# Kernel optimization log

Hardware: AMD Instinct MI355X
Metric: run time of the kernel (lower is better)

The kernel has to match this reference:

```python
import jax, jax.numpy as jnp
from jax import lax
import numpy as np

EPS = 1e-06


def _box_filter(x, radius):
    # Depthwise box mean with zero padding (matches F.conv2d padding=radius),
    # implemented separably: O(r) per pixel instead of O(r^2).
    C = x.shape[1]
    k = 2 * radius + 1
    dn = ('NCHW', 'OIHW', 'NCHW')
    kern_h = jnp.ones((C, 1, k, 1), x.dtype)
    kern_w = jnp.ones((C, 1, 1, k), x.dtype) / (k * k)
    y = lax.conv_general_dilated(x, kern_h, (1, 1), [(radius, radius), (0, 0)],
                                 feature_group_count=C, dimension_numbers=dn)
    return lax.conv_general_dilated(y, kern_w, (1, 1), [(0, 0), (radius, radius)],
                                    feature_group_count=C, dimension_numbers=dn)


def setup_inputs() -> dict:
    key = jax.random.key(0)
    k1, k2 = jax.random.split(key)
    I = jax.random.uniform(k1, (8, 1, 1024, 1024), dtype=jnp.float32)
    p = jax.random.uniform(k2, (8, 3, 1024, 1024), dtype=jnp.float32)
    return {"I": I, "p": p, "radius": 3}


def reference(I, p, radius):
    mean_I = _box_filter(I, radius)            # (B,1,H,W)
    mean_p = _box_filter(p, radius)            # (B,3,H,W)
    mean_Ip = _box_filter(I * p, radius)
    mean_II = _box_filter(I * I, radius)
    cov_Ip = mean_Ip - mean_I * mean_p
    var_I = mean_II - mean_I * mean_I
    a = cov_Ip / (var_I + EPS)
    b = mean_p - a * mean_I
    mean_a = _box_filter(a, radius)
    mean_b = _box_filter(b, radius)
    q = mean_a * I + mean_b
    return jnp.clip(q, 0.0, 1.0)
```

## Files before the change

### kernel.cpp

```cpp
#include <hip/hip_runtime.h>


typedef float v4 __attribute__((ext_vector_type(4)));
typedef float v2 __attribute__((ext_vector_type(2)));

#define TPB   64
#define OUTW  116
#define SEGH  32
#define HW    1024
#define NIDX  68
#define EPSF  1e-6f
#define INV49 (1.0f/49.0f)

struct St {
    v4 s14[2], s58[2];
    v4 t64[2]; v2 t62[2];
    v4 rab4[8][2]; v2 rab2[8][2];
    v2 rI[8];
    v4 ent[2][2];
    v2 lvp[3], lvpN[3];
};

template<int U>
__device__ __forceinline__ void rowStep(
    St& S, const int r, const int Yb, const int t, const int xc2,
    const bool ok0, const bool ok1, const bool sok, const int x0,
    const float* __restrict__ Ip, const float* __restrict__ P0,
    const float* __restrict__ P1, const float* __restrict__ P2,
    float* __restrict__ Q0, float* __restrict__ Q1, float* __restrict__ Q2,
    v4 (* __restrict__ c8)[2][2][NIDX],
    v4 (* __restrict__ c6A)[2][NIDX],
    v2 (* __restrict__ c6B)[2][NIDX])
{
    constexpr int SU  = U & 1;
    constexpr int WS  = U;
    constexpr int LS  = (U + 1) & 7;
    constexpr int IOS = (U + 2) & 7;

    {
        const v4 cE0 = S.ent[SU][0], cE1 = S.ent[SU][1];
        const v2 LI  = S.rI[LS];
        {
            const float Lx = LI.x;
            const float L0 = S.lvp[0].x, L1 = S.lvp[1].x, L2 = S.lvp[2].x;
            v4 d14, d58;
            d14.x = cE0.x - Lx;
            d14.y = cE0.x*cE0.x - Lx*Lx;
            d14.z = cE0.y - L0;
            d14.w = cE0.z - L1;
            d58.x = cE0.w - L2;
            d58.y = cE0.x*cE0.y - Lx*L0;
            d58.z = cE0.x*cE0.z - Lx*L1;
            d58.w = cE0.x*cE0.w - Lx*L2;
            S.s14[0] += d14; S.s58[0] += d58;
            c8[SU][0][0][t+2] = S.s14[0];
            c8[SU][0][1][t+2] = S.s58[0];
        }
        {
            const float Lx = LI.y;
            const float L0 = S.lvp[0].y, L1 = S.lvp[1].y, L2 = S.lvp[2].y;
            v4 d14, d58;
            d14.x = cE1.x - Lx;
            d14.y = cE1.x*cE1.x - Lx*Lx;
            d14.z = cE1.y - L0;
            d14.w = cE1.z - L1;
            d58.x = cE1.w - L2;
            d58.y = cE1.x*cE1.y - Lx*L0;
            d58.z = cE1.x*cE1.z - Lx*L1;
            d58.w = cE1.x*cE1.w - Lx*L2;
            S.s14[1] += d14; S.s58[1] += d58;
            c8[SU][1][0][t+2] = S.s14[1];
            c8[SU][1][1][t+2] = S.s58[1];
        }
        v2 nI; nI.x = cE0.x; nI.y = cE1.x;
        S.rI[WS] = nI;
    }
    asm volatile("" ::: "memory");

    {
        const v4 e14_1 = c8[SU][0][0][t+1], e14_2 = c8[SU][0][0][t+2],
                 e14_3 = c8[SU][0][0][t+3], e14_4 = c8[SU][0][0][t+4];
        const v4 o14_0 = c8[SU][1][0][t+0], o14_1 = c8[SU][1][0][t+1],
                 o14_2 = c8[SU][1][0][t+2], o14_3 = c8[SU][1][0][t+3];
        const v4 w14 = (e14_1 + e14_2 + e14_3) + (o14_1 + o14_2 + o14_3);
        v4 W14[2]; W14[0] = w14 + o14_0; W14[1] = w14 + e14_4;

        const v4 e58_1 = c8[SU][0][1][t+1], e58_2 = c8[SU][0][1][t+2],
                 e58_3 = c8[SU][0][1][t+3], e58_4 = c8[SU][0][1][t+4];
        const v4 o58_0 = c8[SU][1][1][t+0], o58_1 = c8[SU][1][1][t+1],
                 o58_2 = c8[SU][1][1][t+2], o58_3 = c8[SU][1][1][t+3];
        const v4 w58 = (e58_1 + e58_2 + e58_3) + (o58_1 + o58_2 + o58_3);
        v4 W58[2]; W58[0] = w58 + o58_0; W58[1] = w58 + e58_4;

        const int  yc   = Yb + r - 3;
        const bool ycok = (unsigned)yc < HW;
        const bool okc[2] = {ok0, ok1};
        #pragma unroll
        for (int c = 0; c < 2; ++c) {
            const v4 A = W14[c], B = W58[c];
            const float mi  = A.x * INV49;
            const float mii = A.y * INV49;
            const float rv  = __builtin_amdgcn_rcpf(mii - mi*mi + EPSF);
            const bool abok = ycok && okc[c];
            const float mp0 = A.z*INV49, mp1 = A.w*INV49, mp2 = B.x*INV49;
            const float a0 = (B.y*INV49 - mi*mp0)*rv;
            const float a1 = (B.z*INV49 - mi*mp1)*rv;
            const float a2 = (B.w*INV49 - mi*mp2)*rv;
            const float b0 = fmaf(-a0, mi, mp0);
            const float b1 = fmaf(-a1, mi, mp1);
            const float b2 = fmaf(-a2, mi, mp2);
            v4 ab4; ab4.x = abok?a0:0.f; ab4.y = abok?b0:0.f;
                    ab4.z = abok?a1:0.f; ab4.w = abok?b1:0.f;
            v2 ab2; ab2.x = abok?a2:0.f; ab2.y = abok?b2:0.f;
            S.t64[c] += ab4 - S.rab4[LS][c];  S.rab4[WS][c] = ab4;
            S.t62[c] += ab2 - S.rab2[LS][c];  S.rab2[WS][c] = ab2;
            c6A[SU][c][t+2] = S.t64[c];
            c6B[SU][c][t+2] = S.t62[c];
        }
    }
    asm volatile("" ::: "memory");

    {
        const int yE = Yb + r + 2;
        if (r <= 41 && (unsigned)yE < HW) {
            const size_t ro = (size_t)yE * HW + xc2;
            const v2 vI = *(const v2*)(Ip + ro);
            const v2 va = *(const v2*)(P0 + ro);
            const v2 vb = *(const v2*)(P1 + ro);
            const v2 vc = *(const v2*)(P2 + ro);
            v4 E0, E1;
            E0.x = ok0?vI.x:0.f; E0.y = ok0?va.x:0.f; E0.z = ok0?vb.x:0.f; E0.w = ok0?vc.x:0.f;
            E1.x = ok1?vI.y:0.f; E1.y = ok1?va.y:0.f; E1.z = ok1?vb.y:0.f; E1.w = ok1?vc.y:0.f;
            S.ent[SU][0] = E0; S.ent[SU][1] = E1;
        } else {
            const v4 z = {0.f,0.f,0.f,0.f};
            S.ent[SU][0] = z; S.ent[SU][1] = z;
        }
        const int yL = Yb + r - 6;
        if (r >= 6 && r <= 42 && (unsigned)yL < HW) {
            const size_t ro = (size_t)yL * HW + xc2;
            const v2 va = *(const v2*)(P0 + ro);
            const v2 vb = *(const v2*)(P1 + ro);
            const v2 vc = *(const v2*)(P2 + ro);
            v2 L0, L1v, L2v;
            L0.x  = ok0?va.x:0.f; L0.y  = ok1?va.y:0.f;
            L1v.x = ok0?vb.x:0.f; L1v.y = ok1?vb.y:0.f;
            L2v.x = ok0?vc.x:0.f; L2v.y = ok1?vc.y:0.f;
            S.lvpN[0] = L0; S.lvpN[1] = L1v; S.lvpN[2] = L2v;
        } else {
            const v2 z = {0.f,0.f};
            S.lvpN[0] = z; S.lvpN[1] = z; S.lvpN[2] = z;
        }
    }

    if ((unsigned)(r - 12) <= 31u) {
        const v4 eA1 = c6A[SU][0][t+1], eA2 = c6A[SU][0][t+2],
                 eA3 = c6A[SU][0][t+3], eA4 = c6A[SU][0][t+4];
        const v4 oA0 = c6A[SU][1][t+0], oA1 = c6A[SU][1][t+1],
                 oA2 = c6A[SU][1][t+2], oA3 = c6A[SU][1][t+3];
        const v2 eB1 = c6B[SU][0][t+1], eB2 = c6B[SU][0][t+2],
                 eB3 = c6B[SU][0][t+3], eB4 = c6B[SU][0][t+4];
        const v2 oB0 = c6B[SU][1][t+0], oB1 = c6B[SU][1][t+1],
                 oB2 = c6B[SU][1][t+2], oB3 = c6B[SU][1][t+3];
        const v4 wA = (eA1+eA2+eA3) + (oA1+oA2+oA3);
        const v2 wB = (eB1+eB2+eB3) + (oB1+oB2+oB3);
        const v4 A0 = wA + oA0, A1 = wA + eA4;
        const v2 B0 = wB + oB0, B1 = wB + eB4;
        if (sok) {
            const v2 io = S.rI[IOS];
            const int o = Yb + r - 6;
            const size_t ob = (size_t)o * HW + x0;
            v2 q;
            q.x = fminf(fmaxf(fmaf(A0.x*INV49, io.x, A0.y*INV49), 0.f), 1.f);
            q.y = fminf(fmaxf(fmaf(A1.x*INV49, io.y, A1.y*INV49), 0.f), 1.f);
            *(v2*)(Q0 + ob) = q;
            q.x = fminf(fmaxf(fmaf(A0.z*INV49, io.x, A0.w*INV49), 0.f), 1.f);
            q.y = fminf(fmaxf(fmaf(A1.z*INV49, io.y, A1.w*INV49), 0.f), 1.f);
            *(v2*)(Q1 + ob) = q;
            q.x = fminf(fmaxf(fmaf(B0.x*INV49, io.x, B0.y*INV49), 0.f), 1.f);
            q.y = fminf(fmaxf(fmaf(B1.x*INV49, io.y, B1.y*INV49), 0.f), 1.f);
            *(v2*)(Q2 + ob) = q;
        }
    }
    S.lvp[0] = S.lvpN[0]; S.lvp[1] = S.lvpN[1]; S.lvp[2] = S.lvpN[2];
}

__global__ __launch_bounds__(TPB, 2) void gf_kernel(
    const float* __restrict__ I, const float* __restrict__ P,
    float* __restrict__ Q)
{
    __shared__ v4 c8[2][2][2][NIDX];
    __shared__ v4 c6A[2][2][NIDX];
    __shared__ v2 c6B[2][2][NIDX];

    const int s   = blockIdx.x;
    const int seg = blockIdx.y;
    const int b   = blockIdx.z;
    const int t   = threadIdx.x;

    const int Yb = seg*SEGH - 6;
    const int x0 = s*OUTW - 6 + 2*t;
    const int x1 = x0 + 1;
    const bool ok0 = (unsigned)x0 < HW;
    const bool ok1 = (unsigned)x1 < HW;
    const int  xc2 = min(max(x0, 0), HW-2);
    const bool sok = (t >= 3) && (t <= 60) && ok0 && ok1;

    const float* Ip = I + (size_t)b*HW*HW;
    const float* P0 = P + ((size_t)b*3 + 0)*HW*HW;
    const float* P1 = P + ((size_t)b*3 + 1)*HW*HW;
    const float* P2 = P + ((size_t)b*3 + 2)*HW*HW;
    float* Q0 = Q + ((size_t)b*3 + 0)*HW*HW;
    float* Q1 = Q + ((size_t)b*3 + 1)*HW*HW;
    float* Q2 = Q + ((size_t)b*3 + 2)*HW*HW;

    {
        const v4 z4 = {0.f,0.f,0.f,0.f};
        const v2 z2 = {0.f,0.f};
        v4* a = (v4*)c8;
        for (int i = t; i < 2*2*2*NIDX; i += TPB) a[i] = z4;
        v4* bb = (v4*)c6A;
        for (int i = t; i < 2*2*NIDX; i += TPB) bb[i] = z4;
        v2* cc = (v2*)c6B;
        for (int i = t; i < 2*2*NIDX; i += TPB) cc[i] = z2;
    }

    St S;
    {
        const v4 z4 = {0.f,0.f,0.f,0.f};
        const v2 z2 = {0.f,0.f};
        #pragma unroll
        for (int c = 0; c < 2; ++c) {
            S.s14[c] = z4; S.s58[c] = z4; S.t64[c] = z4; S.t62[c] = z2;
            #pragma unroll
            for (int i = 0; i < 8; ++i) { S.rab4[i][c] = z4; S.rab2[i][c] = z2; }
        }
        #pragma unroll
        for (int i = 0; i < 8; ++i) S.rI[i] = z2;
        S.lvp[0] = z2; S.lvp[1] = z2; S.lvp[2] = z2;
        S.lvpN[0] = z2; S.lvpN[1] = z2; S.lvpN[2] = z2;
        #pragma unroll
        for (int pr = 0; pr < 2; ++pr) {
            const int yE = Yb + pr;
            if ((unsigned)yE < HW) {
                const size_t ro = (size_t)yE * HW + xc2;
                const v2 vI = *(const v2*)(Ip + ro);
                const v2 va = *(const v2*)(P0 + ro);
                const v2 vb = *(const v2*)(P1 + ro);
                const v2 vc = *(const v2*)(P2 + ro);
                v4 E0, E1;
                E0.x = ok0?vI.x:0.f; E0.y = ok0?va.x:0.f; E0.z = ok0?vb.x:0.f; E0.w = ok0?vc.x:0.f;
                E1.x = ok1?vI.y:0.f; E1.y = ok1?va.y:0.f; E1.z = ok1?vb.y:0.f; E1.w = ok1?vc.y:0.f;
                S.ent[pr][0] = E0; S.ent[pr][1] = E1;
            } else {
                S.ent[pr][0] = z4; S.ent[pr][1] = z4;
            }
        }
    }
    __syncthreads();

    for (int m = 0; m < 5; ++m) {
        const int r0 = m*8;
        rowStep<0>(S, r0+0, Yb, t, xc2, ok0, ok1, sok, x0, Ip,P0,P1,P2, Q0,Q1,Q2, c8,c6A,c6B);
        rowStep<1>(S, r0+1, Yb, t, xc2, ok0, ok1, sok, x0, Ip,P0,P1,P2, Q0,Q1,Q2, c8,c6A,c6B);
        rowStep<2>(S, r0+2, Yb, t, xc2, ok0, ok1, sok, x0, Ip,P0,P1,P2, Q0,Q1,Q2, c8,c6A,c6B);
        rowStep<3>(S, r0+3, Yb, t, xc2, ok0, ok1, sok, x0, Ip,P0,P1,P2, Q0,Q1,Q2, c8,c6A,c6B);
        rowStep<4>(S, r0+4, Yb, t, xc2, ok0, ok1, sok, x0, Ip,P0,P1,P2, Q0,Q1,Q2, c8,c6A,c6B);
        rowStep<5>(S, r0+5, Yb, t, xc2, ok0, ok1, sok, x0, Ip,P0,P1,P2, Q0,Q1,Q2, c8,c6A,c6B);
        rowStep<6>(S, r0+6, Yb, t, xc2, ok0, ok1, sok, x0, Ip,P0,P1,P2, Q0,Q1,Q2, c8,c6A,c6B);
        rowStep<7>(S, r0+7, Yb, t, xc2, ok0, ok1, sok, x0, Ip,P0,P1,P2, Q0,Q1,Q2, c8,c6A,c6B);
    }
    rowStep<0>(S, 40, Yb, t, xc2, ok0, ok1, sok, x0, Ip,P0,P1,P2, Q0,Q1,Q2, c8,c6A,c6B);
    rowStep<1>(S, 41, Yb, t, xc2, ok0, ok1, sok, x0, Ip,P0,P1,P2, Q0,Q1,Q2, c8,c6A,c6B);
    rowStep<2>(S, 42, Yb, t, xc2, ok0, ok1, sok, x0, Ip,P0,P1,P2, Q0,Q1,Q2, c8,c6A,c6B);
    rowStep<3>(S, 43, Yb, t, xc2, ok0, ok1, sok, x0, Ip,P0,P1,P2, Q0,Q1,Q2, c8,c6A,c6B);
}

extern "C" void kernel_launch(void* const* d_in, const int* in_sizes, int n_in,
                              void* d_out, int out_size, void* d_ws, size_t ws_size,
                              hipStream_t stream) {
    const float* I = (const float*)d_in[0];
    const float* P = (const float*)d_in[1];
    float* Q = (float*)d_out;

    dim3 grid(9, 32, 8);
    gf_kernel<<<grid, TPB, 0, stream>>>(I, P, Q);
}
```

Before: 309.1 us.

## Process row pairs per step and specialize interior blocks without bounds checks

Rebuilds the row loop so each step handles two rows. It runs both horizontal-sum phases, then issues the global loads for two upcoming rows together, then runs both a/b phases and both output phases. This halves the number of compiler barriers and batches loads so more memory latency overlaps with compute. A templated interior path removes the edge masking and clamping for blocks away from the image borders. The cost is more registers (double-buffered leading-row state) and two instantiated copies of the kernel body, which could push register pressure past the two-wave launch bound.

```diff
diff --git a/kernel.cpp b/kernel.cpp
--- a/kernel.cpp
+++ b/kernel.cpp
@@ -18,171 +18,235 @@
     v4 rab4[8][2]; v2 rab2[8][2];
     v2 rI[8];
     v4 ent[2][2];
-    v2 lvp[3], lvpN[3];
+    v2 lvp[2][3], lvpN[2][3];
 };
 
-template<int U>
-__device__ __forceinline__ void rowStep(
-    St& S, const int r, const int Yb, const int t, const int xc2,
-    const bool ok0, const bool ok1, const bool sok, const int x0,
-    const float* __restrict__ Ip, const float* __restrict__ P0,
-    const float* __restrict__ P1, const float* __restrict__ P2,
-    float* __restrict__ Q0, float* __restrict__ Q1, float* __restrict__ Q2,
-    v4 (* __restrict__ c8)[2][2][NIDX],
-    v4 (* __restrict__ c6A)[2][NIDX],
+struct Ctx {
+    const float *Ip, *P0, *P1, *P2;
+    float *Q0, *Q1, *Q2;
+    int t, x0, xc2, Yb;
+    bool ok0, ok1, sok;
+};
+
+template<int RS, int Q, bool INT>
+__device__ __forceinline__ void phA(St& S, const Ctx& C,
+    v4 (* __restrict__ c8)[2][2][NIDX])
+{
+    constexpr int WS = RS & 7, LS = (RS+1)&7;
+    const v4 cE0 = S.ent[Q][0], cE1 = S.ent[Q][1];
+    const v2 LI  = S.rI[LS];
+    {
+        const float Lx = LI.x;
+        const float L0 = S.lvp[Q][0].x, L1 = S.lvp[Q][1].x, L2 = S.lvp[Q][2].x;
+        v4 d14, d58;
+        d14.x = cE0.x - Lx;
+        d14.y = cE0.x*cE0.x - Lx*Lx;
+        d14.z = cE0.y - L0;
+        d14.w = cE0.z - L1;
+        d58.x = cE0.w - L2;
+        d58.y = cE0.x*cE0.y - Lx*L0;
+        d58.z = cE0.x*cE0.z - Lx*L1;
+        d58.w = cE0.x*cE0.w - Lx*L2;
+        S.s14[0] += d14; S.s58[0] += d58;
+        c8[Q][0][0][C.t+2] = S.s14[0];
+        c8[Q][0][1][C.t+2] = S.s58[0];
+    }
+    {
+        const float Lx = LI.y;
+        const float L0 = S.lvp[Q][0].y, L1 = S.lvp[Q][1].y, L2 = S.lvp[Q][2].y;
+        v4 d14, d58;
+        d14.x = cE1.x - Lx;
+        d14.y = cE1.x*cE1.x - Lx*Lx;
+        d14.z = cE1.y - L0;
+        d14.w = cE1.z - L1;
+        d58.x = cE1.w - L2;
+        d58.y = cE1.x*cE1.y - Lx*L0;
+        d58.z = cE1.x*cE1.z - Lx*L1;
+        d58.w = cE1.x*cE1.w - Lx*L2;
+        S.s14[1] += d14; S.s58[1] += d58;
+        c8[Q][1][0][C.t+2] = S.s14[1];
+        c8[Q][1][1][C.t+2] = S.s58[1];
+    }
+    v2 nI; nI.x = cE0.x; nI.y = cE1.x;
+    S.rI[WS] = nI;
+}
+
+template<int RS, int Q, bool INT>
+__device__ __forceinline__ void phB(St& S, const Ctx& C, const int yc,
+    v4 (* __restrict__ c8)[2][2][NIDX], v4 (* __restrict__ c6A)[2][NIDX],
     v2 (* __restrict__ c6B)[2][NIDX])
 {
-    constexpr int SU  = U & 1;
-    constexpr int WS  = U;
-    constexpr int LS  = (U + 1) & 7;
-    constexpr int IOS = (U + 2) & 7;
-
-    {
-        const v4 cE0 = S.ent[SU][0], cE1 = S.ent[SU][1];
-        const v2 LI  = S.rI[LS];
-        {
-            const float Lx = LI.x;
-            const float L0 = S.lvp[0].x, L1 = S.lvp[1].x, L2 = S.lvp[2].x;
-            v4 d14, d58;
-            d14.x = cE0.x - Lx;
-            d14.y = cE0.x*cE0.x - Lx*Lx;
-            d14.z = cE0.y - L0;
-            d14.w = cE0.z - L1;
-            d58.x = cE0.w - L2;
-            d58.y = cE0.x*cE0.y - Lx*L0;
-            d58.z = cE0.x*cE0.z - Lx*L1;
-            d58.w = cE0.x*cE0.w - Lx*L2;
-            S.s14[0] += d14; S.s58[0] += d58;
-            c8[SU][0][0][t+2] = S.s14[0];
-            c8[SU][0][1][t+2] = S.s58[0];
-        }
-        {
-            const float Lx = LI.y;
-            const float L0 = S.lvp[0].y, L1 = S.lvp[1].y, L2 = S.lvp[2].y;
-            v4 d14, d58;
-            d14.x = cE1.x - Lx;
-            d14.y = cE1.x*cE1.x - Lx*Lx;
-            d14.z = cE1.y - L0;
-            d14.w = cE1.z - L1;
-            d58.x = cE1.w - L2;
-            d58.y = cE1.x*cE1.y - Lx*L0;
-            d58.z = cE1.x*cE1.z - Lx*L1;
-            d58.w = cE1.x*cE1.w - Lx*L2;
-            S.s14[1] += d14; S.s58[1] += d58;
-            c8[SU][1][0][t+2] = S.s14[1];
-            c8[SU][1][1][t+2] = S.s58[1];
-        }
-        v2 nI; nI.x = cE0.x; nI.y = cE1.x;
-        S.rI[WS] = nI;
+    constexpr int WS = RS & 7, LS = (RS+1)&7;
+    const int t = C.t;
+    const v4 e14_1 = c8[Q][0][0][t+1], e14_2 = c8[Q][0][0][t+2],
+             e14_3 = c8[Q][0][0][t+3], e14_4 = c8[Q][0][0][t+4];
+    const v4 o14_0 = c8[Q][1][0][t+0], o14_1 = c8[Q][1][0][t+1],
+             o14_2 = c8[Q][1][0][t+2], o14_3 = c8[Q][1][0][t+3];
+    const v4 w14 = (e14_1 + e14_2 + e14_3) + (o14_1 + o14_2 + o14_3);
+    v4 W14[2]; W14[0] = w14 + o14_0; W14[1] = w14 + e14_4;
+
+    const v4 e58_1 = c8[Q][0][1][t+1], e58_2 = c8[Q][0][1][t+2],
+             e58_3 = c8[Q][0][1][t+3], e58_4 = c8[Q][0][1][t+4];
+    const v4 o58_0 = c8[Q][1][1][t+0], o58_1 = c8[Q][1][1][t+1],
+             o58_2 = c8[Q][1][1][t+2], o58_3 = c8[Q][1][1][t+3];
+    const v4 w58 = (e58_1 + e58_2 + e58_3) + (o58_1 + o58_2 + o58_3);
+    v4 W58[2]; W58[0] = w58 + o58_0; W58[1] = w58 + e58_4;
+
+    const bool ycok = INT ? true : ((unsigned)yc < HW);
+    const bool okc[2] = {C.ok0, C.ok1};
+    #pragma unroll
+    for (int c = 0; c < 2; ++c) {
+        const v4 A = W14[c], B = W58[c];
+        const float mi  = A.x * INV49;
+        const float mii = A.y * INV49;
+        const float rv  = __builtin_amdgcn_rcpf(mii - mi*mi + EPSF);
+        const float mp0 = A.z*INV49, mp1 = A.w*INV49, mp2 = B.x*INV49;
+        const float a0 = (B.y*INV49 - mi*mp0)*rv;
+        const float a1 = (B.z*INV49 - mi*mp1)*rv;
+        const float a2 = (B.w*INV49 - mi*mp2)*rv;
+        const float b0 = fmaf(-a0, mi, mp0);
+        const float b1 = fmaf(-a1, mi, mp1);
+        const float b2 = fmaf(-a2, mi, mp2);
+        v4 ab4; v2 ab2;
+        if constexpr (INT) {
+            ab4.x = a0; ab4.y = b0; ab4.z = a1; ab4.w = b1;
+            ab2.x = a2; ab2.y = b2;
+        } else {
+            const bool abok = ycok && okc[c];
+            ab4.x = abok?a0:0.f; ab4.y = abok?b0:0.f;
+            ab4.z = abok?a1:0.f; ab4.w = abok?b1:0.f;
+            ab2.x = abok?a2:0.f; ab2.y = abok?b2:0.f;
+        }
+        S.t64[c] += ab4 - S.rab4[LS][c];  S.rab4[WS][c] = ab4;
+        S.t62[c] += ab2 - S.rab2[LS][c];  S.rab2[WS][c] = ab2;
+        c6A[Q][c][t+2] = S.t64[c];
+        c6B[Q][c][t+2] = S.t62[c];
+    }
+}
+
+template<int RS, int Q, bool INT>
+__device__ __forceinline__ void phD(St& S, const Ctx& C, const int o,
+    v4 (* __restrict__ c6A)[2][NIDX], v2 (* __restrict__ c6B)[2][NIDX])
+{
+    constexpr int IOS = (RS+2)&7;
+    const int t = C.t;
+    const v4 eA1 = c6A[Q][0][t+1], eA2 = c6A[Q][0][t+2],
+             eA3 = c6A[Q][0][t+3], eA4 = c6A[Q][0][t+4];
+    const v4 oA0 = c6A[Q][1][t+0], oA1 = c6A[Q][1][t+1],
+             oA2 = c6A[Q][1][t+2], oA3 = c6A[Q][1][t+3];
+    const v2 eB1 = c6B[Q][0][t+1], eB2 = c6B[Q][0][t+2],
+             eB3 = c6B[Q][0][t+3], eB4 = c6B[Q][0][t+4];
+    const v2 oB0 = c6B[Q][1][t+0], oB1 = c6B[Q][1][t+1],
+             oB2 = c6B[Q][1][t+2], oB3 = c6B[Q][1][t+3];
+    const v4 wA = (eA1+eA2+eA3) + (oA1+oA2+oA3);
+    const v2 wB = (eB1+eB2+eB3) + (oB1+oB2+oB3);
+    const v4 A0 = wA + oA0, A1 = wA + eA4;
+    const v2 B0 = wB + oB0, B1 = wB + eB4;
+    if (C.sok) {
+        const v2 io = S.rI[IOS];
+        const size_t ob = (size_t)o * HW + C.x0;
+        v2 q;
+        q.x = fminf(fmaxf(fmaf(A0.x*INV49, io.x, A0.y*INV49), 0.f), 1.f);
+        q.y = fminf(fmaxf(fmaf(A1.x*INV49, io.y, A1.y*INV49), 0.f), 1.f);
+        *(v2*)(C.Q0 + ob) = q;
+        q.x = fminf(fmaxf(fmaf(A0.z*INV49, io.x, A0.w*INV49), 0.f), 1.f);
+        q.y = fminf(fmaxf(fmaf(A1.z*INV49, io.y, A1.w*INV49), 0.f), 1.f);
+        *(v2*)(C.Q1 + ob) = q;
+        q.x = fminf(fmaxf(fmaf(B0.x*INV49, io.x, B0.y*INV49), 0.f), 1.f);
+        q.y = fminf(fmaxf(fmaf(B1.x*INV49, io.y, B1.y*INV49), 0.f), 1.f);
+        *(v2*)(C.Q2 + ob) = q;
+    }
+}
+
+template<int U, bool INT>
+__device__ __forceinline__ void batchStep(St& S, const Ctx& C, const int rb,
+    v4 (* __restrict__ c8)[2][2][NIDX], v4 (* __restrict__ c6A)[2][NIDX],
+    v2 (* __restrict__ c6B)[2][NIDX])
+{
+    phA<U,   0, INT>(S, C, c8);
+    phA<U+1, 1, INT>(S, C, c8);
+
+    if (rb <= 40) {
+        #pragma unroll
+        for (int q = 0; q < 2; ++q) {
+            const int yE = C.Yb + rb + 2 + q;
+            if (INT || (unsigned)yE < HW) {
+                const size_t ro = (size_t)yE*HW + (size_t)(INT ? C.x0 : C.xc2);
+                const v2 vI = *(const v2*)(C.Ip + ro);
+                const v2 va = *(const v2*)(C.P0 + ro);
+                const v2 vb = *(const v2*)(C.P1 + ro);
+                const v2 vc = *(const v2*)(C.P2 + ro);
+                v4 E0, E1;
+                if constexpr (INT) {
+                    E0.x=vI.x; E0.y=va.x; E0.z=vb.x; E0.w=vc.x;
+                    E1.x=vI.y; E1.y=va.y; E1.z=vb.y; E1.w=vc.y;
+                } else {
+                    E0.x=C.ok0?vI.x:0.f; E0.y=C.ok0?va.x:0.f;
+                    E0.z=C.ok0?vb.x:0.f; E0.w=C.ok0?vc.x:0.f;
+                    E1.x=C.ok1?vI.y:0.f; E1.y=C.ok1?va.y:0.f;
+                    E1.z=C.ok1?vb.y:0.f; E1.w=C.ok1?vc.y:0.f;
+                }
+                S.ent[q][0] = E0; S.ent[q][1] = E1;
+            } else {
+                const v4 z = {0.f,0.f,0.f,0.f};
+                S.ent[q][0] = z; S.ent[q][1] = z;
+            }
+        }
+        #pragma unroll
+        for (int q = 0; q < 2; ++q) {
+            const int R2 = rb + 2 + q;
+            const int yL = C.Yb + R2 - 7;
+            if (R2 >= 7 && (INT || (unsigned)yL < HW)) {
+                const size_t ro = (size_t)yL*HW + (size_t)(INT ? C.x0 : C.xc2);
+                const v2 va = *(const v2*)(C.P0 + ro);
+                const v2 vb = *(const v2*)(C.P1 + ro);
+                const v2 vc = *(const v2*)(C.P2 + ro);
+                if constexpr (INT) {
+                    S.lvpN[q][0] = va; S.lvpN[q][1] = vb; S.lvpN[q][2] = vc;
+                } else {
+                    v2 L0, L1, L2;
+                    L0.x = C.ok0?va.x:0.f; L0.y = C.ok1?va.y:0.f;
+                    L1.x = C.ok0?vb.x:0.f; L1.y = C.ok1?vb.y:0.f;
+                    L2.x = C.ok0?vc.x:0.f; L2.y = C.ok1?vc.y:0.f;
+                    S.lvpN[q][0] = L0; S.lvpN[q][1] = L1; S.lvpN[q][2] = L2;
+                }
+            } else {
+                const v2 z = {0.f,0.f};
+                S.lvpN[q][0] = z; S.lvpN[q][1] = z; S.lvpN[q][2] = z;
+            }
+        }
     }
     asm volatile("" ::: "memory");
 
-    {
-        const v4 e14_1 = c8[SU][0][0][t+1], e14_2 = c8[SU][0][0][t+2],
-                 e14_3 = c8[SU][0][0][t+3], e14_4 = c8[SU][0][0][t+4];
-        const v4 o14_0 = c8[SU][1][0][t+0], o14_1 = c8[SU][1][0][t+1],
-                 o14_2 = c8[SU][1][0][t+2], o14_3 = c8[SU][1][0][t+3];
-        const v4 w14 = (e14_1 + e14_2 + e14_3) + (o14_1 + o14_2 + o14_3);
-        v4 W14[2]; W14[0] = w14 + o14_0; W14[1] = w14 + e14_4;
-
-        const v4 e58_1 = c8[SU][0][1][t+1], e58_2 = c8[SU][0][1][t+2],
-                 e58_3 = c8[SU][0][1][t+3], e58_4 = c8[SU][0][1][t+4];
-        const v4 o58_0 = c8[SU][1][1][t+0], o58_1 = c8[SU][1][1][t+1],
-                 o58_2 = c8[SU][1][1][t+2], o58_3 = c8[SU][1][1][t+3];
-        const v4 w58 = (e58_1 + e58_2 + e58_3) + (o58_1 + o58_2 + o58_3);
-        v4 W58[2]; W58[0] = w58 + o58_0; W58[1] = w58 + e58_4;
-
-        const int  yc   = Yb + r - 3;
-        const bool ycok = (unsigned)yc < HW;
-        const bool okc[2] = {ok0, ok1};
-        #pragma unroll
-        for (int c = 0; c < 2; ++c) {
-            const v4 A = W14[c], B = W58[c];
-            const float mi  = A.x * INV49;
-            const float mii = A.y * INV49;
-            const float rv  = __builtin_amdgcn_rcpf(mii - mi*mi + EPSF);
-            const bool abok = ycok && okc[c];
-            const float mp0 = A.z*INV49, mp1 = A.w*INV49, mp2 = B.x*INV49;
-            const float a0 = (B.y*INV49 - mi*mp0)*rv;
-            const float a1 = (B.z*INV49 - mi*mp1)*rv;
-            const float a2 = (B.w*INV49 - mi*mp2)*rv;
-            const float b0 = fmaf(-a0, mi, mp0);
-            const float b1 = fmaf(-a1, mi, mp1);
-            const float b2 = fmaf(-a2, mi, mp2);
-            v4 ab4; ab4.x = abok?a0:0.f; ab4.y = abok?b0:0.f;
-                    ab4.z = abok?a1:0.f; ab4.w = abok?b1:0.f;
-            v2 ab2; ab2.x = abok?a2:0.f; ab2.y = abok?b2:0.f;
-            S.t64[c] += ab4 - S.rab4[LS][c];  S.rab4[WS][c] = ab4;
-            S.t62[c] += ab2 - S.rab2[LS][c];  S.rab2[WS][c] = ab2;
-            c6A[SU][c][t+2] = S.t64[c];
-            c6B[SU][c][t+2] = S.t62[c];
-        }
-    }
-    asm volatile("" ::: "memory");
-
-    {
-        const int yE = Yb + r + 2;
-        if (r <= 41 && (unsigned)yE < HW) {
-            const size_t ro = (size_t)yE * HW + xc2;
-            const v2 vI = *(const v2*)(Ip + ro);
-            const v2 va = *(const v2*)(P0 + ro);
-            const v2 vb = *(const v2*)(P1 + ro);
-            const v2 vc = *(const v2*)(P2 + ro);
-            v4 E0, E1;
-            E0.x = ok0?vI.x:0.f; E0.y = ok0?va.x:0.f; E0.z = ok0?vb.x:0.f; E0.w = ok0?vc.x:0.f;
-            E1.x = ok1?vI.y:0.f; E1.y = ok1?va.y:0.f; E1.z = ok1?vb.y:0.f; E1.w = ok1?vc.y:0.f;
-            S.ent[SU][0] = E0; S.ent[SU][1] = E1;
-        } else {
-            const v4 z = {0.f,0.f,0.f,0.f};
-            S.ent[SU][0] = z; S.ent[SU][1] = z;
-        }
-        const int yL = Yb + r - 6;
-        if (r >= 6 && r <= 42 && (unsigned)yL < HW) {
-            const size_t ro = (size_t)yL * HW + xc2;
-            const v2 va = *(const v2*)(P0 + ro);
-            const v2 vb = *(const v2*)(P1 + ro);
-            const v2 vc = *(const v2*)(P2 + ro);
-            v2 L0, L1v, L2v;
-            L0.x  = ok0?va.x:0.f; L0.y  = ok1?va.y:0.f;
-            L1v.x = ok0?vb.x:0.f; L1v.y = ok1?vb.y:0.f;
-            L2v.x = ok0?vc.x:0.f; L2v.y = ok1?vc.y:0.f;
-            S.lvpN[0] = L0; S.lvpN[1] = L1v; S.lvpN[2] = L2v;
-        } else {
-            const v2 z = {0.f,0.f};
-            S.lvpN[0] = z; S.lvpN[1] = z; S.lvpN[2] = z;
-        }
-    }
-
-    if ((unsigned)(r - 12) <= 31u) {
-        const v4 eA1 = c6A[SU][0][t+1], eA2 = c6A[SU][0][t+2],
-                 eA3 = c6A[SU][0][t+3], eA4 = c6A[SU][0][t+4];
-        const v4 oA0 = c6A[SU][1][t+0], oA1 = c6A[SU][1][t+1],
-                 oA2 = c6A[SU][1][t+2], oA3 = c6A[SU][1][t+3];
-        const v2 eB1 = c6B[SU][0][t+1], eB2 = c6B[SU][0][t+2],
-                 eB3 = c6B[SU][0][t+3], eB4 = c6B[SU][0][t+4];
-        const v2 oB0 = c6B[SU][1][t+0], oB1 = c6B[SU][1][t+1],
-                 oB2 = c6B[SU][1][t+2], oB3 = c6B[SU][1][t+3];
-        const v4 wA = (eA1+eA2+eA3) + (oA1+oA2+oA3);
-        const v2 wB = (eB1+eB2+eB3) + (oB1+oB2+oB3);
-        const v4 A0 = wA + oA0, A1 = wA + eA4;
-        const v2 B0 = wB + oB0, B1 = wB + eB4;
-        if (sok) {
-            const v2 io = S.rI[IOS];
-            const int o = Yb + r - 6;
-            const size_t ob = (size_t)o * HW + x0;
-            v2 q;
-            q.x = fminf(fmaxf(fmaf(A0.x*INV49, io.x, A0.y*INV49), 0.f), 1.f);
-            q.y = fminf(fmaxf(fmaf(A1.x*INV49, io.y, A1.y*INV49), 0.f), 1.f);
-            *(v2*)(Q0 + ob) = q;
-            q.x = fminf(fmaxf(fmaf(A0.z*INV49, io.x, A0.w*INV49), 0.f), 1.f);
-            q.y = fminf(fmaxf(fmaf(A1.z*INV49, io.y, A1.w*INV49), 0.f), 1.f);
-            *(v2*)(Q1 + ob) = q;
-            q.x = fminf(fmaxf(fmaf(B0.x*INV49, io.x, B0.y*INV49), 0.f), 1.f);
-            q.y = fminf(fmaxf(fmaf(B1.x*INV49, io.y, B1.y*INV49), 0.f), 1.f);
-            *(v2*)(Q2 + ob) = q;
-        }
-    }
-    S.lvp[0] = S.lvpN[0]; S.lvp[1] = S.lvpN[1]; S.lvp[2] = S.lvpN[2];
+    phB<U,   0, INT>(S, C, C.Yb + rb - 3, c8, c6A, c6B);
+    phB<U+1, 1, INT>(S, C, C.Yb + rb - 2, c8, c6A, c6B);
+
+    if (rb >= 12) {
+        phD<U,   0, INT>(S, C, C.Yb + rb - 6, c6A, c6B);
+        phD<U+1, 1, INT>(S, C, C.Yb + rb - 5, c6A, c6B);
+    }
+    #pragma unroll
+    for (int q = 0; q < 2; ++q) {
+        S.lvp[q][0] = S.lvpN[q][0];
+        S.lvp[q][1] = S.lvpN[q][1];
+        S.lvp[q][2] = S.lvpN[q][2];
+    }
+}
+
+template<bool INT>
+__device__ __forceinline__ void mainLoop(St& S, const Ctx& C,
+    v4 (* __restrict__ c8)[2][2][NIDX], v4 (* __restrict__ c6A)[2][NIDX],
+    v2 (* __restrict__ c6B)[2][NIDX])
+{
+    for (int m = 0; m < 5; ++m) {
+        const int rb = m*8;
+        batchStep<0, INT>(S, C, rb,   c8, c6A, c6B);
+        batchStep<2, INT>(S, C, rb+2, c8, c6A, c6B);
+        batchStep<4, INT>(S, C, rb+4, c8, c6A, c6B);
+        batchStep<6, INT>(S, C, rb+6, c8, c6A, c6B);
+    }
+    batchStep<0, INT>(S, C, 40, c8, c6A, c6B);
+    batchStep<2, INT>(S, C, 42, c8, c6A, c6B);
 }
 
 __global__ __launch_bounds__(TPB, 2) void gf_kernel(
@@ -198,21 +262,22 @@
     const int b   = blockIdx.z;
     const int t   = threadIdx.x;
 
-    const int Yb = seg*SEGH - 6;
-    const int x0 = s*OUTW - 6 + 2*t;
-    const int x1 = x0 + 1;
-    const bool ok0 = (unsigned)x0 < HW;
-    const bool ok1 = (unsigned)x1 < HW;
-    const int  xc2 = min(max(x0, 0), HW-2);
-    const bool sok = (t >= 3) && (t <= 60) && ok0 && ok1;
-
-    const float* Ip = I + (size_t)b*HW*HW;
-    const float* P0 = P + ((size_t)b*3 + 0)*HW*HW;
-    const float* P1 = P + ((size_t)b*3 + 1)*HW*HW;
-    const float* P2 = P + ((size_t)b*3 + 2)*HW*HW;
-    float* Q0 = Q + ((size_t)b*3 + 0)*HW*HW;
-    float* Q1 = Q + ((size_t)b*3 + 1)*HW*HW;
-    float* Q2 = Q + ((size_t)b*3 + 2)*HW*HW;
+    Ctx C;
+    C.t  = t;
+    C.Yb = seg*SEGH - 6;
+    C.x0 = s*OUTW - 6 + 2*t;
+    const int x1 = C.x0 + 1;
+    C.ok0 = (unsigned)C.x0 < HW;
+    C.ok1 = (unsigned)x1   < HW;
+    C.xc2 = min(max(C.x0, 0), HW-2);
+    C.sok = (t >= 3) && (t <= 60) && C.ok0 && C.ok1;
+    C.Ip = I + (size_t)b*HW*HW;
+    C.P0 = P + ((size_t)b*3 + 0)*HW*HW;
+    C.P1 = P + ((size_t)b*3 + 1)*HW*HW;
+    C.P2 = P + ((size_t)b*3 + 2)*HW*HW;
+    C.Q0 = Q + ((size_t)b*3 + 0)*HW*HW;
+    C.Q1 = Q + ((size_t)b*3 + 1)*HW*HW;
+    C.Q2 = Q + ((size_t)b*3 + 2)*HW*HW;
 
     {
         const v4 z4 = {0.f,0.f,0.f,0.f};
@@ -237,43 +302,36 @@
         }
         #pragma unroll
         for (int i = 0; i < 8; ++i) S.rI[i] = z2;
-        S.lvp[0] = z2; S.lvp[1] = z2; S.lvp[2] = z2;
-        S.lvpN[0] = z2; S.lvpN[1] = z2; S.lvpN[2] = z2;
-        #pragma unroll
-        for (int pr = 0; pr < 2; ++pr) {
-            const int yE = Yb + pr;
+        #pragma unroll
+        for (int q = 0; q < 2; ++q) {
+            S.lvp[q][0]=z2; S.lvp[q][1]=z2; S.lvp[q][2]=z2;
+            S.lvpN[q][0]=z2; S.lvpN[q][1]=z2; S.lvpN[q][2]=z2;
+        }
+        #pragma unroll
+        for (int q = 0; q < 2; ++q) {
+            const int yE = C.Yb + q;
             if ((unsigned)yE < HW) {
-                const size_t ro = (size_t)yE * HW + xc2;
-                const v2 vI = *(const v2*)(Ip + ro);
-                const v2 va = *(const v2*)(P0 + ro);
-                const v2 vb = *(const v2*)(P1 + ro);
-                const v2 vc = *(const v2*)(P2 + ro);
+                const size_t ro = (size_t)yE * HW + C.xc2;
+                const v2 vI = *(const v2*)(C.Ip + ro);
+                const v2 va = *(const v2*)(C.P0 + ro);
+                const v2 vb = *(const v2*)(C.P1 + ro);
+                const v2 vc = *(const v2*)(C.P2 + ro);
                 v4 E0, E1;
-                E0.x = ok0?vI.x:0.f; E0.y = ok0?va.x:0.f; E0.z = ok0?vb.x:0.f; E0.w = ok0?vc.x:0.f;
-                E1.x = ok1?vI.y:0.f; E1.y = ok1?va.y:0.f; E1.z = ok1?vb.y:0.f; E1.w = ok1?vc.y:0.f;
-                S.ent[pr][0] = E0; S.ent[pr][1] = E1;
+                E0.x=C.ok0?vI.x:0.f; E0.y=C.ok0?va.x:0.f;
+                E0.z=C.ok0?vb.x:0.f; E0.w=C.ok0?vc.x:0.f;
+                E1.x=C.ok1?vI.y:0.f; E1.y=C.ok1?va.y:0.f;
+                E1.z=C.ok1?vb.y:0.f; E1.w=C.ok1?vc.y:0.f;
+                S.ent[q][0] = E0; S.ent[q][1] = E1;
             } else {
-                S.ent[pr][0] = z4; S.ent[pr][1] = z4;
+                S.ent[q][0] = z4; S.ent[q][1] = z4;
             }
         }
     }
     __syncthreads();
 
-    for (int m = 0; m < 5; ++m) {
-        const int r0 = m*8;
-        rowStep<0>(S, r0+0, Yb, t, xc2, ok0, ok1, sok, x0, Ip,P0,P1,P2, Q0,Q1,Q2, c8,c6A,c6B);
-        rowStep<1>(S, r0+1, Yb, t, xc2, ok0, ok1, sok, x0, Ip,P0,P1,P2, Q0,Q1,Q2, c8,c6A,c6B);
-        rowStep<2>(S, r0+2, Yb, t, xc2, ok0, ok1, sok, x0, Ip,P0,P1,P2, Q0,Q1,Q2, c8,c6A,c6B);
-        rowStep<3>(S, r0+3, Yb, t, xc2, ok0, ok1, sok, x0, Ip,P0,P1,P2, Q0,Q1,Q2, c8,c6A,c6B);
-        rowStep<4>(S, r0+4, Yb, t, xc2, ok0, ok1, sok, x0, Ip,P0,P1,P2, Q0,Q1,Q2, c8,c6A,c6B);
-        rowStep<5>(S, r0+5, Yb, t, xc2, ok0, ok1, sok, x0, Ip,P0,P1,P2, Q0,Q1,Q2, c8,c6A,c6B);
-        rowStep<6>(S, r0+6, Yb, t, xc2, ok0, ok1, sok, x0, Ip,P0,P1,P2, Q0,Q1,Q2, c8,c6A,c6B);
-        rowStep<7>(S, r0+7, Yb, t, xc2, ok0, ok1, sok, x0, Ip,P0,P1,P2, Q0,Q1,Q2, c8,c6A,c6B);
-    }
-    rowStep<0>(S, 40, Yb, t, xc2, ok0, ok1, sok, x0, Ip,P0,P1,P2, Q0,Q1,Q2, c8,c6A,c6B);
-    rowStep<1>(S, 41, Yb, t, xc2, ok0, ok1, sok, x0, Ip,P0,P1,P2, Q0,Q1,Q2, c8,c6A,c6B);
-    rowStep<2>(S, 42, Yb, t, xc2, ok0, ok1, sok, x0, Ip,P0,P1,P2, Q0,Q1,Q2, c8,c6A,c6B);
-    rowStep<3>(S, 43, Yb, t, xc2, ok0, ok1, sok, x0, Ip,P0,P1,P2, Q0,Q1,Q2, c8,c6A,c6B);
+    const bool interior = (s >= 1) && (s <= 7) && (seg >= 1) && (seg <= 30);
+    if (interior) mainLoop<true >(S, C, c8, c6A, c6B);
+    else          mainLoop<false>(S, C, c8, c6A, c6B);
 }
 
 extern "C" void kernel_launch(void* const* d_in, const int* in_sizes, int n_in,
```

New measurement: 295.0 us. 1.05x faster.
